# Kernel optimization log

Measured on AMD Instinct MI355X. Metric: run time of the kernel, lower is better.

Reference implementation:

```python
import jax, jax.numpy as jnp
import numpy as np

B, T = 32, 4096
QD, MD, AD = 1024, 512, 128
F, K = 32, 31
PAD = (K - 1) // 2  # 'same' padding as in Tacotron-2 location conv


def setup_inputs() -> dict:
    key = jax.random.key(0)
    ks = jax.random.split(key, 12)
    s = lambda fan_in: 1.0 / np.sqrt(fan_in)
    return {
        "query": jax.random.normal(ks[0], (B, QD), jnp.float32),
        "memory": jax.random.normal(ks[1], (B, T, MD), jnp.float32),
        "alignments": jax.random.uniform(ks[2], (B, T, 2), jnp.float32),
        "mask": jnp.zeros((B, T), dtype=bool),
        "Wq": jax.random.normal(ks[3], (QD, AD), jnp.float32) * s(QD),
        "bq": jnp.zeros((AD,), jnp.float32),
        "Wm": jax.random.normal(ks[4], (MD, AD), jnp.float32) * s(MD),
        "bm": jnp.zeros((AD,), jnp.float32),
        "conv_w": jax.random.normal(ks[5], (F, 2, K), jnp.float32) * s(2 * K),
        "conv_b": jnp.zeros((F,), jnp.float32),
        "Wl": jax.random.normal(ks[6], (F, AD), jnp.float32) * s(F),
        "bl": jnp.zeros((AD,), jnp.float32),
        "v_w": jax.random.normal(ks[7], (AD,), jnp.float32) * s(AD),
        "v_b": jnp.zeros((), jnp.float32),
    }


def reference(query, memory, alignments, mask, Wq, bq, Wm, bm, conv_w, conv_b, Wl, bl, v_w, v_b):
    # processed memory: [B, T, AD]
    processed_memory = jnp.einsum("btm,ma->bta", memory, Wm) + bm
    # processed query: [B, 1, AD] (query.unsqueeze(1))
    processed_query = (query @ Wq + bq)[:, None, :]
    # location features: conv over time on [B, 2, T] -> [B, F, T]
    a = jnp.transpose(alignments, (0, 2, 1))  # [B, 2, T]
    loc = jax.lax.conv_general_dilated(
        a, conv_w, window_strides=(1,), padding=[(PAD, PAD)],
        dimension_numbers=("NCH", "OIH", "NCH"))
    loc = loc + conv_b[None, :, None]
    loc = jnp.transpose(loc, (0, 2, 1))  # [B, T, F]
    processed_loc = jnp.einsum("btf,fa->bta", loc, Wl) + bl
    # additive score: v . tanh(q + m + l)  -> [B, T]
    score = jnp.einsum("bta,a->bt", jnp.tanh(processed_query + processed_memory + processed_loc), v_w) + v_b
    score = jnp.where(mask, -jnp.inf, score)
    alignment = jax.nn.softmax(score, axis=-1)  # [B, T]
    context = jnp.einsum("bt,btm->bm", alignment, memory)  # [B, MD]
    return context, alignment
```

## Files before the change

kernel.cpp:

```cpp
#include <hip/hip_runtime.h>
#include <hip/hip_bf16.h>
#include <math.h>

#define B_ 32
#define T_ 4096
#define QD_ 1024
#define MD_ 512
#define AD_ 128
#define F_ 32
#define K_ 31
#define PAD_ 15

#define TT 64
#define NBLK (T_ / TT)

typedef float f32x16 __attribute__((ext_vector_type(16)));
typedef unsigned int uint4v __attribute__((ext_vector_type(4)));

__device__ inline unsigned pk_bf2(float lo, float hi) {
    unsigned ul = __float_as_uint(lo) + 0x8000u;
    unsigned uh = __float_as_uint(hi) + 0x8000u;
    return __builtin_amdgcn_perm(uh, ul, 0x07060302u);
}

__device__ inline unsigned short f2bf_rn(float f) {
    unsigned u = __float_as_uint(f);
    u += 0x7fffu + ((u >> 16) & 1u);
    return (unsigned short)(u >> 16);
}

__device__ inline float bf2f(unsigned short u) {
    return __uint_as_float(((unsigned)u) << 16);
}

__device__ inline void mfma32(f32x16& c, uint4v a, uint4v b) {
    asm("s_nop 1\n\tv_mfma_f32_32x32x16_bf16 %0, %1, %2, %0"
        : "+v"(c) : "v"(a), "v"(b));
}

__global__ __launch_bounds__(256) void k_prep(const float* __restrict__ Wm,
                                              unsigned short* __restrict__ wmT_sw) {
    int gid = blockIdx.x * 256 + threadIdx.x;
    int kk = gid >> 8;
    int ct = (gid >> 6) & 3;
    int lane = gid & 63;
    int k0 = kk * 16 + (lane >> 5) * 8;
    int a = ct * 32 + (lane & 31);
    unsigned short o[8];
#pragma unroll
    for (int j = 0; j < 8; j++) o[j] = f2bf_rn(Wm[(k0 + j) * AD_ + a]);
    uint4v v;
    v[0] = ((unsigned)o[1] << 16) | o[0];
    v[1] = ((unsigned)o[3] << 16) | o[2];
    v[2] = ((unsigned)o[5] << 16) | o[4];
    v[3] = ((unsigned)o[7] << 16) | o[6];
    *(uint4v*)(wmT_sw + (long)gid * 8) = v;
}

__global__ __launch_bounds__(128) void k_pq(const float* __restrict__ query,
                                            const float* __restrict__ Wq,
                                            float* __restrict__ pq) {
    int b = blockIdx.x;
    int qc = blockIdx.y;
    int a = threadIdx.x;
    const float* qrow = query + b * QD_ + qc * 128;
    const float* wq = Wq + (qc * 128) * AD_ + a;
    float acc = 0.f;
#pragma unroll 4
    for (int i = 0; i < 128; i++) acc += qrow[i] * wq[i * AD_];
    atomicAdd(&pq[b * AD_ + a], acc);
}

__global__ __launch_bounds__(256, 4) void k_score_ctx(
    const float* __restrict__ memory, const float* __restrict__ alignments,
    const unsigned char* __restrict__ mask,
    const unsigned short* __restrict__ wmT_sw, const float* __restrict__ bm,
    const float* __restrict__ convw, const float* __restrict__ convb,
    const float* __restrict__ Wl, const float* __restrict__ bl,
    const float* __restrict__ vw, const float* __restrict__ vb,
    const float* __restrict__ pq, const float* __restrict__ bq,
    float* __restrict__ scores, float* __restrict__ bmax,
    float* __restrict__ bden, float* __restrict__ num) {
    __shared__ __align__(16) unsigned short s_base[TT * AD_];
    __shared__ __align__(16) unsigned char s_u[16896];
    __shared__ float s_score[TT];
    __shared__ float s_w[TT];

    const int tid = threadIdx.x;
    const int b = blockIdx.y;
    const int blk = blockIdx.x;
    const int t0 = blk * TT;

    float* convw_s = (float*)s_u;
    float* align_s = convw_s + 1984;
    float* loc_s   = align_s + 192;
    unsigned short* sab = (unsigned short*)s_u;

    if (tid < TT) s_score[tid] = 0.f;

    for (int i = tid; i < F_ * 2 * K_; i += 256) convw_s[i] = convw[i];
    for (int i = tid; i < (TT + K_ - 1) * 2; i += 256) {
        int tg = t0 + (i >> 1) - PAD_;
        align_s[i] = (tg >= 0 && tg < T_) ? alignments[((long)b * T_ + tg) * 2 + (i & 1)] : 0.f;
    }
    __syncthreads();

    for (int i = tid; i < TT * F_; i += 256) {
        int f = i & (F_ - 1);
        int t = i >> 5;
        float acc = convb[f];
        const float* w0 = &convw_s[f * (2 * K_)];
        const float* w1 = w0 + K_;
        const float* al = &align_s[t * 2];
#pragma unroll
        for (int k = 0; k < K_; k++) acc += al[2 * k] * w0[k] + al[2 * k + 1] * w1[k];
        loc_s[t * F_ + f] = acc;
    }
    __syncthreads();

    for (int i = tid; i < TT * AD_; i += 256) {
        int a = i & (AD_ - 1);
        int t = i >> 7;
        float acc = pq[b * AD_ + a] + bq[a] + bm[a] + bl[a];
        const float* lrow = &loc_s[t * F_];
#pragma unroll
        for (int f = 0; f < F_; f++) acc += lrow[f] * Wl[f * AD_ + a];
        s_base[i] = f2bf_rn(acc);
    }
    __syncthreads();

    const int lane = tid & 63;
    const int w = tid >> 6;
    const int rt = w >> 1;
    const int ct0 = (w & 1) * 2;
    const int half = lane >> 5;
    const int l31 = lane & 31;

    const int srow = tid >> 3;
    const int skq = (tid & 7) * 4;
    const float* aptr = memory + ((long)b * T_ + t0) * MD_;
    const float* g_lo = aptr + srow * MD_ + skq;
    const float* g_hi = aptr + (srow + 32) * MD_ + skq;
    unsigned short* w_lo[2], * w_hi[2];
    w_lo[0] = sab + srow * 40 + skq;          w_hi[0] = sab + (srow + 32) * 40 + skq;
    w_lo[1] = w_lo[0] + 2560;                 w_hi[1] = w_hi[0] + 2560;

    const unsigned short* bptr = wmT_sw + ((long)ct0 * 64 + lane) * 8;
    const int arow = (rt * 32 + l31) * 40 + half * 8;

    f32x16 c0, c1;
#pragma unroll
    for (int i = 0; i < 16; i++) { c0[i] = 0.f; c1[i] = 0.f; }

    float4 A0 = *(const float4*)(g_lo);
    float4 A1 = *(const float4*)(g_hi);
    uint4v B00 = *(const uint4v*)(bptr);
    uint4v B01 = *(const uint4v*)(bptr + 512);
    uint4v B10 = *(const uint4v*)(bptr + 2048);
    uint4v B11 = *(const uint4v*)(bptr + 2048 + 512);
    ((unsigned*)w_lo[0])[0] = pk_bf2(A0.x, A0.y);
    ((unsigned*)w_lo[0])[1] = pk_bf2(A0.z, A0.w);
    ((unsigned*)w_hi[0])[0] = pk_bf2(A1.x, A1.y);
    ((unsigned*)w_hi[0])[1] = pk_bf2(A1.z, A1.w);
    __syncthreads();

    for (int c = 0; c < 16; c++) {
        const int cb = c & 1, nb = cb ^ 1;
        float4 N0, N1;
        uint4v NB00, NB01, NB10, NB11;
        {
            int kcn = (c < 15) ? (c + 1) * 32 : 0;
            N0 = *(const float4*)(g_lo + kcn);
            N1 = *(const float4*)(g_hi + kcn);
            long kkn = (c < 15) ? (long)(2 * c + 2) * 2048 : 0;
            NB00 = *(const uint4v*)(bptr + kkn);
            NB01 = *(const uint4v*)(bptr + kkn + 512);
            NB10 = *(const uint4v*)(bptr + kkn + 2048);
            NB11 = *(const uint4v*)(bptr + kkn + 2048 + 512);
        }
        uint4v af0 = *(const uint4v*)(sab + cb * 2560 + arow);
        uint4v af1 = *(const uint4v*)(sab + cb * 2560 + arow + 16);
        mfma32(c0, af0, B00);
        mfma32(c1, af0, B01);
        mfma32(c0, af1, B10);
        mfma32(c1, af1, B11);
        B00 = NB00; B01 = NB01; B10 = NB10; B11 = NB11;
        if (c < 15) {
            ((unsigned*)w_lo[nb])[0] = pk_bf2(N0.x, N0.y);
            ((unsigned*)w_lo[nb])[1] = pk_bf2(N0.z, N0.w);
            ((unsigned*)w_hi[nb])[0] = pk_bf2(N1.x, N1.y);
            ((unsigned*)w_hi[nb])[1] = pk_bf2(N1.z, N1.w);
        }
        __syncthreads();
    }
    asm volatile("s_nop 7\n\ts_nop 7\n\ts_nop 7" ::: "memory");

    float vwa0 = vw[ct0 * 32 + l31];
    float vwa1 = vw[ct0 * 32 + 32 + l31];
#pragma unroll
    for (int i = 0; i < 16; i++) {
        int t = rt * 32 + (i & 3) + 8 * (i >> 2) + 4 * half;
        float b0 = bf2f(s_base[t * AD_ + ct0 * 32 + l31]);
        float b1 = bf2f(s_base[t * AD_ + ct0 * 32 + 32 + l31]);
        float s = tanhf(c0[i] + b0) * vwa0 + tanhf(c1[i] + b1) * vwa1;
        s += __shfl_xor(s, 1);
        s += __shfl_xor(s, 2);
        s += __shfl_xor(s, 4);
        s += __shfl_xor(s, 8);
        s += __shfl_xor(s, 16);
        if (l31 == 0) atomicAdd(&s_score[t], s);
    }
    __syncthreads();

    if (tid < TT) {
        float s = s_score[tid] + vb[0];
        bool mk = mask[(long)b * T_ + t0 + tid] != 0;
        if (mk) s = -INFINITY;
        scores[b * T_ + t0 + tid] = s;
        float m = s;
#pragma unroll
        for (int off = 32; off >= 1; off >>= 1) m = fmaxf(m, __shfl_xor(m, off));
        float e = (m == -INFINITY) ? 0.f : expf(s - m);
        float d = e;
#pragma unroll
        for (int off = 32; off >= 1; off >>= 1) d += __shfl_xor(d, off);
        s_w[tid] = e;
        if (tid == 0) {
            bmax[b * NBLK + blk] = m;
            bden[b * NBLK + blk] = d;
        }
    }
    __syncthreads();

    {
        const float2* mp = (const float2*)aptr + tid;
        float ax = 0.f, ay = 0.f;
#pragma unroll 8
        for (int t = 0; t < TT; t++) {
            float2 v = mp[t * 256];
            float wt = s_w[t];
            ax += wt * v.x;
            ay += wt * v.y;
        }
        float2 o; o.x = ax; o.y = ay;
        *(float2*)(num + ((long)b * NBLK + blk) * MD_ + tid * 2) = o;
    }
}

__global__ __launch_bounds__(512) void k_reduce(
    const float* __restrict__ bmax, const float* __restrict__ bden,
    const float* __restrict__ num, const float* __restrict__ scores,
    float* __restrict__ ctx, float* __restrict__ oalign) {
    int b = blockIdx.x;
    int tid = threadIdx.x;
    __shared__ float sm[NBLK], se[NBLK];
    __shared__ float sD;
    if (tid < NBLK) sm[tid] = bmax[b * NBLK + tid];
    __syncthreads();
    float M = -INFINITY;
#pragma unroll
    for (int i = 0; i < NBLK; i++) M = fmaxf(M, sm[i]);
    if (tid < NBLK) se[tid] = expf(sm[tid] - M) * bden[b * NBLK + tid];
    __syncthreads();
    if (tid == 0) {
        float D = 0.f;
        for (int i = 0; i < NBLK; i++) D += se[i];
        sD = D;
    }
    if (tid < NBLK) se[tid] = expf(sm[tid] - M);
    __syncthreads();
    float invD = 1.f / sD;

    float acc = 0.f;
    const float* np = num + (long)b * NBLK * MD_ + tid;
#pragma unroll 8
    for (int blk = 0; blk < NBLK; blk++) acc += se[blk] * np[blk * MD_];
    ctx[b * MD_ + tid] = acc * invD;

    for (int t = tid; t < T_; t += 512) {
        oalign[b * T_ + t] = expf(scores[b * T_ + t] - M) * invD;
    }
}

extern "C" void kernel_launch(void* const* d_in, const int* in_sizes, int n_in,
                              void* d_out, int out_size, void* d_ws, size_t ws_size,
                              hipStream_t stream) {
    const float* query      = (const float*)d_in[0];
    const float* memory     = (const float*)d_in[1];
    const float* alignments = (const float*)d_in[2];
    const unsigned char* mask = (const unsigned char*)d_in[3];
    const float* Wq    = (const float*)d_in[4];
    const float* bq    = (const float*)d_in[5];
    const float* Wm    = (const float*)d_in[6];
    const float* bm    = (const float*)d_in[7];
    const float* convw = (const float*)d_in[8];
    const float* convb = (const float*)d_in[9];
    const float* Wl    = (const float*)d_in[10];
    const float* bl    = (const float*)d_in[11];
    const float* vw    = (const float*)d_in[12];
    const float* vb    = (const float*)d_in[13];

    float* out = (float*)d_out;
    float* ctx = out;
    float* oalign = out + B_ * MD_;

    float* ws = (float*)d_ws;
    float* pq     = ws;
    float* scores = pq + B_ * AD_;
    float* bmax   = scores + B_ * T_;
    float* bden   = bmax + B_ * NBLK;
    float* num    = bden + B_ * NBLK;
    unsigned short* wmT_sw = (unsigned short*)(num + (long)B_ * NBLK * MD_);

    hipMemsetAsync(pq, 0, B_ * AD_ * sizeof(float), stream);

    k_prep<<<32, 256, 0, stream>>>(Wm, wmT_sw);
    k_pq<<<dim3(B_, QD_ / 128), 128, 0, stream>>>(query, Wq, pq);
    k_score_ctx<<<dim3(NBLK, B_), 256, 0, stream>>>(
        memory, alignments, mask, wmT_sw, bm, convw, convb, Wl, bl, vw, vb, pq, bq,
        scores, bmax, bden, num);
    k_reduce<<<B_, 512, 0, stream>>>(bmax, bden, num, scores, ctx, oalign);
}
```

Baseline: 486.2 us.

## Split location-feature kernel out and shrink score kernel to one wave per 32 rows

Moves the location conv and Wl projection into a separate kernel, k_ploc, which writes a bf16 per-timestep base to workspace. The score/context kernel becomes a single 64-thread wave per 32-timestep tile that loads memory rows directly into registers for the MFMAs, with no LDS staging and no block barriers. Unnormalized exp weights are written straight into the alignment output and rescaled in the reduce kernel, which removes the scores buffer. This trades extra global traffic for the ploc tensor (32x4096x128 bf16) and doubled per-block partial sums against higher occupancy and less synchronization.

```diff
diff --git a/kernel.cpp b/kernel.cpp
--- a/kernel.cpp
+++ b/kernel.cpp
@@ -1,5 +1,4 @@
 #include <hip/hip_runtime.h>
-#include <hip/hip_bf16.h>
 #include <math.h>
 
 #define B_ 32
@@ -11,7 +10,7 @@
 #define K_ 31
 #define PAD_ 15
 
-#define TT 64
+#define TT 32
 #define NBLK (T_ / TT)
 
 typedef float f32x16 __attribute__((ext_vector_type(16)));
@@ -71,214 +70,202 @@
     atomicAdd(&pq[b * AD_ + a], acc);
 }
 
-__global__ __launch_bounds__(256, 4) void k_score_ctx(
-    const float* __restrict__ memory, const float* __restrict__ alignments,
-    const unsigned char* __restrict__ mask,
-    const unsigned short* __restrict__ wmT_sw, const float* __restrict__ bm,
-    const float* __restrict__ convw, const float* __restrict__ convb,
-    const float* __restrict__ Wl, const float* __restrict__ bl,
+__global__ __launch_bounds__(256) void k_ploc(
+    const float* __restrict__ alignments, const float* __restrict__ convw,
+    const float* __restrict__ convb, const float* __restrict__ Wl,
+    const float* __restrict__ bl, const float* __restrict__ bm,
+    const float* __restrict__ bq, const float* __restrict__ pq,
+    unsigned short* __restrict__ ploc) {
+    __shared__ float s_cw[F_ * 2 * K_];
+    __shared__ float s_al[(128 + K_ - 1) * 2];
+    __shared__ float s_loc[128 * F_];
+
+    const int tid = threadIdx.x;
+    const int b = blockIdx.y;
+    const int t0 = blockIdx.x * 128;
+
+    for (int i = tid; i < F_ * 2 * K_; i += 256) s_cw[i] = convw[i];
+    for (int i = tid; i < (128 + K_ - 1) * 2; i += 256) {
+        int tg = t0 + (i >> 1) - PAD_;
+        s_al[i] = (tg >= 0 && tg < T_) ? alignments[((long)b * T_ + tg) * 2 + (i & 1)] : 0.f;
+    }
+    __syncthreads();
+
+    for (int i = tid; i < 128 * F_; i += 256) {
+        int f = i & (F_ - 1);
+        int t = i >> 5;
+        float acc = convb[f];
+        const float* w0 = &s_cw[f * (2 * K_)];
+        const float* w1 = w0 + K_;
+        const float2* ap = (const float2*)&s_al[t * 2];
+#pragma unroll
+        for (int k = 0; k < K_; k++) {
+            float2 a2 = ap[k];
+            acc += a2.x * w0[k] + a2.y * w1[k];
+        }
+        s_loc[t * F_ + f] = acc;
+    }
+    __syncthreads();
+
+    const int a = tid & 127;
+    float wl[F_];
+#pragma unroll
+    for (int f = 0; f < F_; f++) wl[f] = Wl[f * AD_ + a];
+    const float base = pq[b * AD_ + a] + bq[a] + bm[a] + bl[a];
+    unsigned short* outp = ploc + ((long)b * T_ + t0) * AD_ + a;
+    for (int t = (tid >> 7); t < 128; t += 2) {
+        float acc = base;
+        const float* lr = &s_loc[t * F_];
+#pragma unroll
+        for (int f = 0; f < F_; f++) acc += lr[f] * wl[f];
+        outp[(long)t * AD_] = f2bf_rn(acc);
+    }
+}
+
+__global__ __launch_bounds__(64) void k_score_ctx(
+    const float* __restrict__ memory, const unsigned char* __restrict__ mask,
+    const unsigned short* __restrict__ wmT_sw, const unsigned short* __restrict__ ploc,
     const float* __restrict__ vw, const float* __restrict__ vb,
-    const float* __restrict__ pq, const float* __restrict__ bq,
-    float* __restrict__ scores, float* __restrict__ bmax,
-    float* __restrict__ bden, float* __restrict__ num) {
-    __shared__ __align__(16) unsigned short s_base[TT * AD_];
-    __shared__ __align__(16) unsigned char s_u[16896];
-    __shared__ float s_score[TT];
-    __shared__ float s_w[TT];
-
-    const int tid = threadIdx.x;
+    float* __restrict__ bmax, float* __restrict__ bden,
+    float* __restrict__ num, float* __restrict__ oalign) {
+    __shared__ __align__(16) float s_sc[TT];
+    __shared__ __align__(16) float s_w[TT];
+
+    const int lane = threadIdx.x;
+    const int l31 = lane & 31;
+    const int h = lane >> 5;
     const int b = blockIdx.y;
     const int blk = blockIdx.x;
     const int t0 = blk * TT;
 
-    float* convw_s = (float*)s_u;
-    float* align_s = convw_s + 1984;
-    float* loc_s   = align_s + 192;
-    unsigned short* sab = (unsigned short*)s_u;
-
-    if (tid < TT) s_score[tid] = 0.f;
-
-    for (int i = tid; i < F_ * 2 * K_; i += 256) convw_s[i] = convw[i];
-    for (int i = tid; i < (TT + K_ - 1) * 2; i += 256) {
-        int tg = t0 + (i >> 1) - PAD_;
-        align_s[i] = (tg >= 0 && tg < T_) ? alignments[((long)b * T_ + tg) * 2 + (i & 1)] : 0.f;
-    }
-    __syncthreads();
-
-    for (int i = tid; i < TT * F_; i += 256) {
-        int f = i & (F_ - 1);
-        int t = i >> 5;
-        float acc = convb[f];
-        const float* w0 = &convw_s[f * (2 * K_)];
-        const float* w1 = w0 + K_;
-        const float* al = &align_s[t * 2];
-#pragma unroll
-        for (int k = 0; k < K_; k++) acc += al[2 * k] * w0[k] + al[2 * k + 1] * w1[k];
-        loc_s[t * F_ + f] = acc;
-    }
-    __syncthreads();
-
-    for (int i = tid; i < TT * AD_; i += 256) {
-        int a = i & (AD_ - 1);
-        int t = i >> 7;
-        float acc = pq[b * AD_ + a] + bq[a] + bm[a] + bl[a];
-        const float* lrow = &loc_s[t * F_];
-#pragma unroll
-        for (int f = 0; f < F_; f++) acc += lrow[f] * Wl[f * AD_ + a];
-        s_base[i] = f2bf_rn(acc);
-    }
-    __syncthreads();
-
-    const int lane = tid & 63;
-    const int w = tid >> 6;
-    const int rt = w >> 1;
-    const int ct0 = (w & 1) * 2;
-    const int half = lane >> 5;
-    const int l31 = lane & 31;
-
-    const int srow = tid >> 3;
-    const int skq = (tid & 7) * 4;
     const float* aptr = memory + ((long)b * T_ + t0) * MD_;
-    const float* g_lo = aptr + srow * MD_ + skq;
-    const float* g_hi = aptr + (srow + 32) * MD_ + skq;
-    unsigned short* w_lo[2], * w_hi[2];
-    w_lo[0] = sab + srow * 40 + skq;          w_hi[0] = sab + (srow + 32) * 40 + skq;
-    w_lo[1] = w_lo[0] + 2560;                 w_hi[1] = w_hi[0] + 2560;
-
-    const unsigned short* bptr = wmT_sw + ((long)ct0 * 64 + lane) * 8;
-    const int arow = (rt * 32 + l31) * 40 + half * 8;
-
-    f32x16 c0, c1;
-#pragma unroll
-    for (int i = 0; i < 16; i++) { c0[i] = 0.f; c1[i] = 0.f; }
-
-    float4 A0 = *(const float4*)(g_lo);
-    float4 A1 = *(const float4*)(g_hi);
-    uint4v B00 = *(const uint4v*)(bptr);
-    uint4v B01 = *(const uint4v*)(bptr + 512);
-    uint4v B10 = *(const uint4v*)(bptr + 2048);
-    uint4v B11 = *(const uint4v*)(bptr + 2048 + 512);
-    ((unsigned*)w_lo[0])[0] = pk_bf2(A0.x, A0.y);
-    ((unsigned*)w_lo[0])[1] = pk_bf2(A0.z, A0.w);
-    ((unsigned*)w_hi[0])[0] = pk_bf2(A1.x, A1.y);
-    ((unsigned*)w_hi[0])[1] = pk_bf2(A1.z, A1.w);
-    __syncthreads();
-
-    for (int c = 0; c < 16; c++) {
-        const int cb = c & 1, nb = cb ^ 1;
-        float4 N0, N1;
-        uint4v NB00, NB01, NB10, NB11;
-        {
-            int kcn = (c < 15) ? (c + 1) * 32 : 0;
-            N0 = *(const float4*)(g_lo + kcn);
-            N1 = *(const float4*)(g_hi + kcn);
-            long kkn = (c < 15) ? (long)(2 * c + 2) * 2048 : 0;
-            NB00 = *(const uint4v*)(bptr + kkn);
-            NB01 = *(const uint4v*)(bptr + kkn + 512);
-            NB10 = *(const uint4v*)(bptr + kkn + 2048);
-            NB11 = *(const uint4v*)(bptr + kkn + 2048 + 512);
-        }
-        uint4v af0 = *(const uint4v*)(sab + cb * 2560 + arow);
-        uint4v af1 = *(const uint4v*)(sab + cb * 2560 + arow + 16);
-        mfma32(c0, af0, B00);
-        mfma32(c1, af0, B01);
-        mfma32(c0, af1, B10);
-        mfma32(c1, af1, B11);
-        B00 = NB00; B01 = NB01; B10 = NB10; B11 = NB11;
-        if (c < 15) {
-            ((unsigned*)w_lo[nb])[0] = pk_bf2(N0.x, N0.y);
-            ((unsigned*)w_lo[nb])[1] = pk_bf2(N0.z, N0.w);
-            ((unsigned*)w_hi[nb])[0] = pk_bf2(N1.x, N1.y);
-            ((unsigned*)w_hi[nb])[1] = pk_bf2(N1.z, N1.w);
-        }
-        __syncthreads();
+    const float* arow = aptr + l31 * MD_ + h * 8;
+    const unsigned short* bpk = wmT_sw + lane * 8;
+
+    f32x16 c0, c1, c2, c3;
+#pragma unroll
+    for (int i = 0; i < 16; i++) { c0[i] = 0.f; c1[i] = 0.f; c2[i] = 0.f; c3[i] = 0.f; }
+
+    for (int cc = 0; cc < 16; ++cc) {
+        const float4 p0 = *(const float4*)(arow + cc * 32);
+        const float4 p1 = *(const float4*)(arow + cc * 32 + 4);
+        const float4 p2 = *(const float4*)(arow + cc * 32 + 16);
+        const float4 p3 = *(const float4*)(arow + cc * 32 + 20);
+        const int kb0 = (2 * cc) * 2048;
+        const int kb1 = kb0 + 2048;
+        uint4v b00 = *(const uint4v*)(bpk + kb0);
+        uint4v b01 = *(const uint4v*)(bpk + kb0 + 512);
+        uint4v b02 = *(const uint4v*)(bpk + kb0 + 1024);
+        uint4v b03 = *(const uint4v*)(bpk + kb0 + 1536);
+        uint4v b10 = *(const uint4v*)(bpk + kb1);
+        uint4v b11 = *(const uint4v*)(bpk + kb1 + 512);
+        uint4v b12 = *(const uint4v*)(bpk + kb1 + 1024);
+        uint4v b13 = *(const uint4v*)(bpk + kb1 + 1536);
+        uint4v af0, af1;
+        af0[0] = pk_bf2(p0.x, p0.y); af0[1] = pk_bf2(p0.z, p0.w);
+        af0[2] = pk_bf2(p1.x, p1.y); af0[3] = pk_bf2(p1.z, p1.w);
+        af1[0] = pk_bf2(p2.x, p2.y); af1[1] = pk_bf2(p2.z, p2.w);
+        af1[2] = pk_bf2(p3.x, p3.y); af1[3] = pk_bf2(p3.z, p3.w);
+        mfma32(c0, af0, b00); mfma32(c1, af0, b01);
+        mfma32(c2, af0, b02); mfma32(c3, af0, b03);
+        mfma32(c0, af1, b10); mfma32(c1, af1, b11);
+        mfma32(c2, af1, b12); mfma32(c3, af1, b13);
     }
     asm volatile("s_nop 7\n\ts_nop 7\n\ts_nop 7" ::: "memory");
 
-    float vwa0 = vw[ct0 * 32 + l31];
-    float vwa1 = vw[ct0 * 32 + 32 + l31];
+    const unsigned short* plp = ploc + ((long)b * T_ + t0) * AD_ + l31;
+    const float vw0 = vw[l31];
+    const float vw1 = vw[32 + l31];
+    const float vw2 = vw[64 + l31];
+    const float vw3 = vw[96 + l31];
 #pragma unroll
     for (int i = 0; i < 16; i++) {
-        int t = rt * 32 + (i & 3) + 8 * (i >> 2) + 4 * half;
-        float b0 = bf2f(s_base[t * AD_ + ct0 * 32 + l31]);
-        float b1 = bf2f(s_base[t * AD_ + ct0 * 32 + 32 + l31]);
-        float s = tanhf(c0[i] + b0) * vwa0 + tanhf(c1[i] + b1) * vwa1;
+        const int row = (i & 3) + 8 * (i >> 2) + 4 * h;
+        const unsigned short* pr = plp + row * AD_;
+        float s = tanhf(c0[i] + bf2f(pr[0]))  * vw0
+                + tanhf(c1[i] + bf2f(pr[32])) * vw1
+                + tanhf(c2[i] + bf2f(pr[64])) * vw2
+                + tanhf(c3[i] + bf2f(pr[96])) * vw3;
         s += __shfl_xor(s, 1);
         s += __shfl_xor(s, 2);
         s += __shfl_xor(s, 4);
         s += __shfl_xor(s, 8);
         s += __shfl_xor(s, 16);
-        if (l31 == 0) atomicAdd(&s_score[t], s);
-    }
-    __syncthreads();
-
-    if (tid < TT) {
-        float s = s_score[tid] + vb[0];
-        bool mk = mask[(long)b * T_ + t0 + tid] != 0;
-        if (mk) s = -INFINITY;
-        scores[b * T_ + t0 + tid] = s;
-        float m = s;
-#pragma unroll
-        for (int off = 32; off >= 1; off >>= 1) m = fmaxf(m, __shfl_xor(m, off));
-        float e = (m == -INFINITY) ? 0.f : expf(s - m);
-        float d = e;
-#pragma unroll
-        for (int off = 32; off >= 1; off >>= 1) d += __shfl_xor(d, off);
-        s_w[tid] = e;
-        if (tid == 0) {
-            bmax[b * NBLK + blk] = m;
-            bden[b * NBLK + blk] = d;
-        }
-    }
-    __syncthreads();
-
-    {
-        const float2* mp = (const float2*)aptr + tid;
-        float ax = 0.f, ay = 0.f;
+        if (l31 == 0) s_sc[row] = s;
+    }
+
+    if (lane < TT) {
+        float s = s_sc[lane] + vb[0];
+        if (mask[(long)b * T_ + t0 + lane]) s = -INFINITY;
+        s_sc[lane] = s;
+    }
+    float m = -INFINITY;
+#pragma unroll
+    for (int r = 0; r < TT; r++) m = fmaxf(m, s_sc[r]);
+    float e = 0.f;
+    if (lane < TT) {
+        e = (m == -INFINITY) ? 0.f : expf(s_sc[lane] - m);
+        s_w[lane] = e;
+        oalign[(long)b * T_ + t0 + lane] = e;
+    }
+    float d = e;
+    d += __shfl_xor(d, 1);
+    d += __shfl_xor(d, 2);
+    d += __shfl_xor(d, 4);
+    d += __shfl_xor(d, 8);
+    d += __shfl_xor(d, 16);
+    if (lane == 0) { bmax[b * NBLK + blk] = m; bden[b * NBLK + blk] = d; }
+
+    const float2* mp = (const float2*)aptr + lane;
+    float2 a0 = make_float2(0.f, 0.f), a1 = make_float2(0.f, 0.f);
+    float2 a2 = make_float2(0.f, 0.f), a3 = make_float2(0.f, 0.f);
 #pragma unroll 8
-        for (int t = 0; t < TT; t++) {
-            float2 v = mp[t * 256];
-            float wt = s_w[t];
-            ax += wt * v.x;
-            ay += wt * v.y;
-        }
-        float2 o; o.x = ax; o.y = ay;
-        *(float2*)(num + ((long)b * NBLK + blk) * MD_ + tid * 2) = o;
-    }
+    for (int t = 0; t < TT; t++) {
+        const float wt = s_w[t];
+        const float2 v0 = mp[t * 256];
+        const float2 v1 = mp[t * 256 + 64];
+        const float2 v2 = mp[t * 256 + 128];
+        const float2 v3 = mp[t * 256 + 192];
+        a0.x += wt * v0.x; a0.y += wt * v0.y;
+        a1.x += wt * v1.x; a1.y += wt * v1.y;
+        a2.x += wt * v2.x; a2.y += wt * v2.y;
+        a3.x += wt * v3.x; a3.y += wt * v3.y;
+    }
+    float2* np = (float2*)(num + ((long)b * NBLK + blk) * MD_) + lane;
+    np[0] = a0; np[64] = a1; np[128] = a2; np[192] = a3;
 }
 
 __global__ __launch_bounds__(512) void k_reduce(
     const float* __restrict__ bmax, const float* __restrict__ bden,
-    const float* __restrict__ num, const float* __restrict__ scores,
+    const float* __restrict__ num,
     float* __restrict__ ctx, float* __restrict__ oalign) {
     int b = blockIdx.x;
     int tid = threadIdx.x;
-    __shared__ float sm[NBLK], se[NBLK];
+    __shared__ float sm[NBLK], sf[NBLK];
     __shared__ float sD;
     if (tid < NBLK) sm[tid] = bmax[b * NBLK + tid];
     __syncthreads();
     float M = -INFINITY;
-#pragma unroll
+#pragma unroll 8
     for (int i = 0; i < NBLK; i++) M = fmaxf(M, sm[i]);
-    if (tid < NBLK) se[tid] = expf(sm[tid] - M) * bden[b * NBLK + tid];
+    if (tid < NBLK) sf[tid] = expf(sm[tid] - M);
     __syncthreads();
     if (tid == 0) {
         float D = 0.f;
-        for (int i = 0; i < NBLK; i++) D += se[i];
+        for (int i = 0; i < NBLK; i++) D += sf[i] * bden[b * NBLK + i];
         sD = D;
     }
-    if (tid < NBLK) se[tid] = expf(sm[tid] - M);
-    __syncthreads();
-    float invD = 1.f / sD;
+    __syncthreads();
+    const float invD = 1.f / sD;
 
     float acc = 0.f;
     const float* np = num + (long)b * NBLK * MD_ + tid;
 #pragma unroll 8
-    for (int blk = 0; blk < NBLK; blk++) acc += se[blk] * np[blk * MD_];
+    for (int blk = 0; blk < NBLK; blk++) acc += sf[blk] * np[blk * MD_];
     ctx[b * MD_ + tid] = acc * invD;
 
     for (int t = tid; t < T_; t += 512) {
-        oalign[b * T_ + t] = expf(scores[b * T_ + t] - M) * invD;
+        oalign[(long)b * T_ + t] *= sf[t >> 5] * invD;
     }
 }
 
@@ -306,18 +293,18 @@
 
     float* ws = (float*)d_ws;
     float* pq     = ws;
-    float* scores = pq + B_ * AD_;
-    float* bmax   = scores + B_ * T_;
+    float* bmax   = pq + B_ * AD_;
     float* bden   = bmax + B_ * NBLK;
     float* num    = bden + B_ * NBLK;
     unsigned short* wmT_sw = (unsigned short*)(num + (long)B_ * NBLK * MD_);
+    unsigned short* ploc   = wmT_sw + (long)8192 * 8;
 
     hipMemsetAsync(pq, 0, B_ * AD_ * sizeof(float), stream);
 
     k_prep<<<32, 256, 0, stream>>>(Wm, wmT_sw);
     k_pq<<<dim3(B_, QD_ / 128), 128, 0, stream>>>(query, Wq, pq);
-    k_score_ctx<<<dim3(NBLK, B_), 256, 0, stream>>>(
-        memory, alignments, mask, wmT_sw, bm, convw, convb, Wl, bl, vw, vb, pq, bq,
-        scores, bmax, bden, num);
-    k_reduce<<<B_, 512, 0, stream>>>(bmax, bden, num, scores, ctx, oalign);
-}
+    k_ploc<<<dim3(T_ / 128, B_), 256, 0, stream>>>(alignments, convw, convb, Wl, bl, bm, bq, pq, ploc);
+    k_score_ctx<<<dim3(NBLK, B_), 64, 0, stream>>>(
+        memory, mask, wmT_sw, ploc, vw, vb, bmax, bden, num, oalign);
+    k_reduce<<<B_, 512, 0, stream>>>(bmax, bden, num, ctx, oalign);
+}
```

After: 557.8 us. +14.7%, slower.
